# Kernel optimization log

Hardware: AMD Instinct MI355X
Metric: run time of the kernel (lower is better)

Reference implementation:

```python
import jax, jax.numpy as jnp
import numpy as np

EPS = 1e-8

def setup_inputs() -> dict:
    key = jax.random.key(0)
    student_output = jax.random.normal(key, (8192, 768), dtype=jnp.float32)
    return {"student_output": student_output}

def reference(student_output) -> jnp.ndarray:
    # KoLeo: -mean(log(nearest-neighbor euclidean distance + eps))
    x = student_output
    n = x.shape[0]
    sq = jnp.sum(x * x, axis=1)                      # [n]
    # squared pairwise distances via Gram matrix: ||xi||^2 + ||xj||^2 - 2 xi.xj
    d2 = sq[:, None] + sq[None, :] - 2.0 * (x @ x.T)  # [n, n]
    d2 = jnp.maximum(d2, 0.0)
    d2 = jnp.where(jnp.eye(n, dtype=bool), jnp.inf, d2)  # exclude self
    # sqrt is monotone, so min(sqrt(d2)) == sqrt(min(d2)) (matches torch cdist+min)
    min_dist = jnp.sqrt(jnp.min(d2, axis=1))          # [n]
    return -jnp.mean(jnp.log(min_dist + EPS))
```

## Files before the change

kernel.cpp:

```cpp
#include <hip/hip_runtime.h>
#include <hip/hip_bf16.h>
#include <math.h>

#define NROWS 8192
#define DIM   768
#define NKB   (DIM / 64)
#define FCH   8192
#define FPAN  (NKB * FCH)
#define NT128 (NROWS / 128)
#define NTILES (NT128 * (NT128 + 1) / 2)
#define PACK8B ((size_t)NT128 * FPAN)

typedef __attribute__((ext_vector_type(4))) float  f32x4;
typedef __attribute__((ext_vector_type(8))) __bf16 bf16x8;
typedef __attribute__((ext_vector_type(4))) __bf16 bf16x4;
typedef __attribute__((ext_vector_type(2))) long   longx2;

__device__ __forceinline__ void gload_lds16(const void* g, void* l) {
  __builtin_amdgcn_global_load_lds(
      (const __attribute__((address_space(1))) void*)g,
      (__attribute__((address_space(3))) void*)l, 16, 0, 0);
}

__global__ __launch_bounds__(256) void koleo_pack8(const float* __restrict__ X,
                                                   float* __restrict__ sq,
                                                   unsigned int* __restrict__ minbits,
                                                   char* __restrict__ xbf) {
  const int row  = blockIdx.x * 4 + (threadIdx.x >> 6);
  const int lane = threadIdx.x & 63;
  const int rb = row >> 7, r = row & 127;
  const float* xr = X + (size_t)row * DIM;
  float s = 0.f;
#pragma unroll
  for (int i = 0; i < 3; ++i) {
    const int c0 = lane * 4 + i * 256;
    f32x4 v = *(const f32x4*)(xr + c0);
    s += v.x * v.x + v.y * v.y + v.z * v.z + v.w * v.w;
    int pk = __builtin_amdgcn_cvt_pk_fp8_f32(v.x, v.y, 0, false);
    pk     = __builtin_amdgcn_cvt_pk_fp8_f32(v.z, v.w, pk, true);
    const int kb = c0 >> 6;
    const int c  = c0 & 63;
    const int ks = c >> 5;
    const int g  = (c >> 3) & 3;
    const int bb = c & 7;
    const int pos = g * 16 + ks * 8 + bb;
    const int off = (r * 64 + pos) ^ (((r >> 1) & 3) << 4);
    *(int*)(xbf + (size_t)rb * FPAN + (size_t)kb * FCH + off) = pk;
  }
#pragma unroll
  for (int m = 32; m >= 1; m >>= 1) s += __shfl_xor(s, m, 64);
  if (lane == 0) {
    sq[row]      = s;
    minbits[row] = 0x7F800000u;
  }
}

__global__ __launch_bounds__(256, 4) void koleo_tile8f(const char* __restrict__ xbf,
                                                       const float* __restrict__ sq,
                                                       unsigned int* __restrict__ minbits) {
  extern __shared__ char lds[];

  const int b = blockIdx.x;
  int ti, tj;
  if (b < 528) {
    int rem = b, rl = 32; ti = 0;
    while (rem >= rl) { rem -= rl; ++ti; --rl; }
    tj = ti + rem;
  } else if (b < 1552) {
    const int q = (b - 528) >> 8, rr = (b - 528) & 255;
    ti = rr >> 3; tj = 32 + q * 8 + (rr & 7);
  } else {
    int rem = b - 1552, rl = 32; ti = 32;
    while (rem >= rl) { rem -= rl; ++ti; --rl; }
    tj = ti + rem;
  }
  const int i0 = ti * 128, j0 = tj * 128;

  const int tid  = threadIdx.x;
  const int lane = tid & 63;
  const int wave = tid >> 6;
  const int wr   = wave >> 1;
  const int wc   = wave & 1;
  const int g16  = (lane >> 4) * 16;

  const char* pA = xbf + (size_t)ti * FPAN + wave * 1024 + lane * 16;
  const char* pB = xbf + (size_t)tj * FPAN + wave * 1024 + lane * 16;

  f32x4 acc[4][4] = {};

#pragma unroll
  for (int h = 0; h < 2; ++h) {
    gload_lds16(pA + h * 4096, lds +        h * 4096 + wave * 1024);
    gload_lds16(pB + h * 4096, lds + 8192 + h * 4096 + wave * 1024);
  }
  asm volatile("s_waitcnt vmcnt(0)" ::: "memory");
  __builtin_amdgcn_s_barrier();

  for (int t = 0; t < NKB; ++t) {
    char* buf  = lds + (t & 1) * 16384;
    char* nbuf = lds + ((t + 1) & 1) * 16384;
    const bool more = (t + 1 < NKB);

    if (more) {
      const char* sA = pA + (size_t)(t + 1) * FCH;
      const char* sB = pB + (size_t)(t + 1) * FCH;
#pragma unroll
      for (int h = 0; h < 2; ++h) {
        gload_lds16(sA + h * 4096, nbuf +        h * 4096 + wave * 1024);
        gload_lds16(sB + h * 4096, nbuf + 8192 + h * 4096 + wave * 1024);
      }
    }

    longx2 aP[4], bP[4];
#pragma unroll
    for (int m = 0; m < 4; ++m) {
      const int ra = wr * 64 + m * 16 + (lane & 15);
      aP[m] = *(const longx2*)(buf + ((ra * 64 + g16) ^ (((ra >> 1) & 3) << 4)));
      const int rb2 = wc * 64 + m * 16 + (lane & 15);
      bP[m] = *(const longx2*)(buf + 8192 + ((rb2 * 64 + g16) ^ (((rb2 >> 1) & 3) << 4)));
    }
#pragma unroll
    for (int ks = 0; ks < 2; ++ks)
#pragma unroll
      for (int m = 0; m < 4; ++m)
#pragma unroll
        for (int n = 0; n < 4; ++n)
          acc[m][n] = __builtin_amdgcn_mfma_f32_16x16x32_fp8_fp8(aP[m][ks], bP[n][ks], acc[m][n], 0, 0, 0);

    if (more) asm volatile("s_waitcnt vmcnt(0)" ::: "memory");
    __builtin_amdgcn_s_barrier();
  }

  const int cg = lane >> 4;
  const int cl = lane & 15;
  float sqj[4], colmin[4];
#pragma unroll
  for (int n = 0; n < 4; ++n) {
    sqj[n]    = sq[j0 + wc * 64 + n * 16 + cl];
    colmin[n] = INFINITY;
  }
#pragma unroll
  for (int m = 0; m < 4; ++m) {
#pragma unroll
    for (int r = 0; r < 4; ++r) {
      const int gi = i0 + wr * 64 + m * 16 + cg * 4 + r;
      const float si = sq[gi];
      float rowmin = INFINITY;
#pragma unroll
      for (int n = 0; n < 4; ++n) {
        const int gj = j0 + wc * 64 + n * 16 + cl;
        float d2 = si + sqj[n] - 2.0f * acc[m][n][r];
        d2 = fmaxf(d2, 0.0f);
        if (gi == gj) d2 = INFINITY;
        rowmin    = fminf(rowmin, d2);
        colmin[n] = fminf(colmin[n], d2);
      }
      rowmin = fminf(rowmin, __shfl_xor(rowmin, 1, 64));
      rowmin = fminf(rowmin, __shfl_xor(rowmin, 2, 64));
      rowmin = fminf(rowmin, __shfl_xor(rowmin, 4, 64));
      rowmin = fminf(rowmin, __shfl_xor(rowmin, 8, 64));
      if (cl == 0)
        atomicMin(minbits + gi, __float_as_uint(rowmin));
    }
  }
  if (ti != tj) {
#pragma unroll
    for (int n = 0; n < 4; ++n) {
      float cm = colmin[n];
      cm = fminf(cm, __shfl_xor(cm, 16, 64));
      cm = fminf(cm, __shfl_xor(cm, 32, 64));
      if (cg == 0)
        atomicMin(minbits + j0 + wc * 64 + n * 16 + cl, __float_as_uint(cm));
    }
  }
}

__global__ __launch_bounds__(256) void koleo_prep_fb(const float* __restrict__ X,
                                                     float* __restrict__ sq,
                                                     unsigned int* __restrict__ minbits) {
  const int row  = blockIdx.x * 4 + (threadIdx.x >> 6);
  const int lane = threadIdx.x & 63;
  const float* xr = X + (size_t)row * DIM;
  float s = 0.f;
#pragma unroll
  for (int i = 0; i < 3; ++i) {
    f32x4 v = *(const f32x4*)(xr + lane * 4 + i * 256);
    s += v.x * v.x + v.y * v.y + v.z * v.z + v.w * v.w;
  }
#pragma unroll
  for (int m = 32; m >= 1; m >>= 1) s += __shfl_xor(s, m, 64);
  if (lane == 0) { sq[row] = s; minbits[row] = 0x7F800000u; }
}

__global__ __launch_bounds__(256) void koleo_tile_fb(const float* __restrict__ X,
                                                     const float* __restrict__ sq,
                                                     unsigned int* __restrict__ minbits) {
  __shared__ __align__(16) char sA[16384];
  __shared__ __align__(16) char sB[16384];
  int rem = blockIdx.x, ti = 0, rowlen = NT128;
  while (rem >= rowlen) { rem -= rowlen; ++ti; --rowlen; }
  const int tj = ti + rem;
  const int i0 = ti * 128, j0 = tj * 128;
  const int tid = threadIdx.x, lane = tid & 63, wave = tid >> 6;
  const int wr = wave >> 1, wc = wave & 1;
  f32x4 acc[4][4] = {};
  for (int k0 = 0; k0 < DIM; k0 += 64) {
    __syncthreads();
#pragma unroll
    for (int it = 0; it < 8; ++it) {
      const int idx = tid + it * 256;
      const int r = idx >> 4, c4 = idx & 15;
      f32x4 va = *(const f32x4*)(X + (size_t)(i0 + r) * DIM + k0 + c4 * 4);
      f32x4 vb = *(const f32x4*)(X + (size_t)(j0 + r) * DIM + k0 + c4 * 4);
      bf16x4 ha, hb;
      ha[0] = (__bf16)va.x; ha[1] = (__bf16)va.y; ha[2] = (__bf16)va.z; ha[3] = (__bf16)va.w;
      hb[0] = (__bf16)vb.x; hb[1] = (__bf16)vb.y; hb[2] = (__bf16)vb.z; hb[3] = (__bf16)vb.w;
      int off = (r * 128 + c4 * 8) ^ ((r & 7) << 4);
      *(bf16x4*)(sA + off) = ha;
      *(bf16x4*)(sB + off) = hb;
    }
    __syncthreads();
#pragma unroll
    for (int ks = 0; ks < 2; ++ks) {
      bf16x8 af[4], bfr[4];
#pragma unroll
      for (int m = 0; m < 4; ++m) {
        const int ra = wr * 64 + m * 16 + (lane & 15);
        af[m]  = *(const bf16x8*)(sA + ((ra * 128 + ks * 64 + (lane >> 4) * 16) ^ ((ra & 7) << 4)));
        const int rb2 = wc * 64 + m * 16 + (lane & 15);
        bfr[m] = *(const bf16x8*)(sB + ((rb2 * 128 + ks * 64 + (lane >> 4) * 16) ^ ((rb2 & 7) << 4)));
      }
#pragma unroll
      for (int m = 0; m < 4; ++m)
#pragma unroll
        for (int n = 0; n < 4; ++n)
          acc[m][n] = __builtin_amdgcn_mfma_f32_16x16x32_bf16(af[m], bfr[n], acc[m][n], 0, 0, 0);
    }
  }
  const int cg = lane >> 4, cl = lane & 15;
  float sqj[4], colmin[4];
#pragma unroll
  for (int n = 0; n < 4; ++n) { sqj[n] = sq[j0 + wc * 64 + n * 16 + cl]; colmin[n] = INFINITY; }
#pragma unroll
  for (int m = 0; m < 4; ++m) {
#pragma unroll
    for (int r = 0; r < 4; ++r) {
      const int gi = i0 + wr * 64 + m * 16 + cg * 4 + r;
      const float si = sq[gi];
      float rowmin = INFINITY;
#pragma unroll
      for (int n = 0; n < 4; ++n) {
        const int gj = j0 + wc * 64 + n * 16 + cl;
        float d2 = si + sqj[n] - 2.0f * acc[m][n][r];
        d2 = fmaxf(d2, 0.0f);
        if (gi == gj) d2 = INFINITY;
        rowmin = fminf(rowmin, d2);
        colmin[n] = fminf(colmin[n], d2);
      }
      rowmin = fminf(rowmin, __shfl_xor(rowmin, 1, 64));
      rowmin = fminf(rowmin, __shfl_xor(rowmin, 2, 64));
      rowmin = fminf(rowmin, __shfl_xor(rowmin, 4, 64));
      rowmin = fminf(rowmin, __shfl_xor(rowmin, 8, 64));
      if (cl == 0) atomicMin(minbits + gi, __float_as_uint(rowmin));
    }
  }
  if (ti != tj) {
#pragma unroll
    for (int n = 0; n < 4; ++n) {
      float cm = colmin[n];
      cm = fminf(cm, __shfl_xor(cm, 16, 64));
      cm = fminf(cm, __shfl_xor(cm, 32, 64));
      if (cg == 0) atomicMin(minbits + j0 + wc * 64 + n * 16 + cl, __float_as_uint(cm));
    }
  }
}

__global__ __launch_bounds__(1024) void koleo_final(const unsigned int* __restrict__ minbits,
                                                    float* __restrict__ out) {
  __shared__ float wsum[16];
  float s = 0.f;
  for (int i = threadIdx.x; i < NROWS; i += 1024) {
    float d2 = __uint_as_float(minbits[i]);
    s += logf(sqrtf(d2) + 1e-8f);
  }
#pragma unroll
  for (int m = 32; m >= 1; m >>= 1) s += __shfl_xor(s, m, 64);
  const int wv = threadIdx.x >> 6, ln = threadIdx.x & 63;
  if (ln == 0) wsum[wv] = s;
  __syncthreads();
  if (wv == 0) {
    float t = (ln < 16) ? wsum[ln] : 0.f;
#pragma unroll
    for (int m = 8; m >= 1; m >>= 1) t += __shfl_xor(t, m, 64);
    if (ln == 0) out[0] = -t / (float)NROWS;
  }
}

extern "C" void kernel_launch(void* const* d_in, const int* in_sizes, int n_in,
                              void* d_out, int out_size, void* d_ws, size_t ws_size,
                              hipStream_t stream) {
  const float* X = (const float*)d_in[0];
  float* out = (float*)d_out;
  unsigned int* minbits = (unsigned int*)d_ws;
  float* sq = (float*)((char*)d_ws + NROWS * sizeof(unsigned int));
  char* xbf = (char*)d_ws + 65536;

  const size_t need = 65536 + PACK8B;
  if (ws_size >= need) {
    koleo_pack8<<<NROWS / 4, 256, 0, stream>>>(X, sq, minbits, xbf);
    koleo_tile8f<<<NTILES, 256, 32768, stream>>>(xbf, sq, minbits);
  } else {
    koleo_prep_fb<<<NROWS / 4, 256, 0, stream>>>(X, sq, minbits);
    koleo_tile_fb<<<NTILES, 256, 0, stream>>>(X, sq, minbits);
  }
  koleo_final<<<1, 1024, 0, stream>>>(minbits, out);
}
```

Before: 65.16 us.

## Enlarge symmetric Gram tiles to 256x256 with 16-wave blocks

```diff
diff --git a/kernel.cpp b/kernel.cpp
--- a/kernel.cpp
+++ b/kernel.cpp
@@ -8,7 +8,8 @@
 #define FCH   8192
 #define FPAN  (NKB * FCH)
 #define NT128 (NROWS / 128)
-#define NTILES (NT128 * (NT128 + 1) / 2)
+#define NT256 (NROWS / 256)
+#define NTIL2 (NT256 * (NT256 + 1) / 2)
 #define PACK8B ((size_t)NT128 * FPAN)
 
 typedef __attribute__((ext_vector_type(4))) float  f32x4;
@@ -55,69 +56,69 @@
   }
 }
 
-__global__ __launch_bounds__(256, 4) void koleo_tile8f(const char* __restrict__ xbf,
-                                                       const float* __restrict__ sq,
-                                                       unsigned int* __restrict__ minbits) {
+__global__ __launch_bounds__(1024, 4) void koleo_tile256(const char* __restrict__ xbf,
+                                                         const float* __restrict__ sq,
+                                                         unsigned int* __restrict__ minbits) {
   extern __shared__ char lds[];
 
   const int b = blockIdx.x;
   int ti, tj;
-  if (b < 528) {
-    int rem = b, rl = 32; ti = 0;
+  if (b < 136) {
+    int rem = b, rl = 16; ti = 0;
     while (rem >= rl) { rem -= rl; ++ti; --rl; }
     tj = ti + rem;
-  } else if (b < 1552) {
-    const int q = (b - 528) >> 8, rr = (b - 528) & 255;
-    ti = rr >> 3; tj = 32 + q * 8 + (rr & 7);
+  } else if (b < 392) {
+    const int q = (b - 136) >> 6, rr = (b - 136) & 63;
+    ti = rr >> 2; tj = 16 + q * 4 + (rr & 3);
   } else {
-    int rem = b - 1552, rl = 32; ti = 32;
+    int rem = b - 392, rl = 16; ti = 16;
     while (rem >= rl) { rem -= rl; ++ti; --rl; }
     tj = ti + rem;
   }
-  const int i0 = ti * 128, j0 = tj * 128;
+  const int i0 = ti * 256, j0 = tj * 256;
 
   const int tid  = threadIdx.x;
   const int lane = tid & 63;
   const int wave = tid >> 6;
-  const int wr   = wave >> 1;
-  const int wc   = wave & 1;
+  const int wr   = wave >> 2;
+  const int wc   = wave & 3;
   const int g16  = (lane >> 4) * 16;
 
-  const char* pA = xbf + (size_t)ti * FPAN + wave * 1024 + lane * 16;
-  const char* pB = xbf + (size_t)tj * FPAN + wave * 1024 + lane * 16;
+  const int sc   = wave >> 2;
+  const int spart= wave & 3;
+  const int srb  = (sc < 2) ? (2 * ti + sc) : (2 * tj + (sc - 2));
+  const char* sbase = xbf + (size_t)srb * FPAN + spart * 2048 + lane * 16;
+  const int sdst = sc * 8192 + spart * 2048;
 
   f32x4 acc[4][4] = {};
 
-#pragma unroll
-  for (int h = 0; h < 2; ++h) {
-    gload_lds16(pA + h * 4096, lds +        h * 4096 + wave * 1024);
-    gload_lds16(pB + h * 4096, lds + 8192 + h * 4096 + wave * 1024);
-  }
+  gload_lds16(sbase,        lds + sdst);
+  gload_lds16(sbase + 1024, lds + sdst + 1024);
   asm volatile("s_waitcnt vmcnt(0)" ::: "memory");
   __builtin_amdgcn_s_barrier();
 
   for (int t = 0; t < NKB; ++t) {
-    char* buf  = lds + (t & 1) * 16384;
-    char* nbuf = lds + ((t + 1) & 1) * 16384;
+    char* buf  = lds + (t & 1) * 32768;
+    char* nbuf = lds + ((t + 1) & 1) * 32768;
     const bool more = (t + 1 < NKB);
 
     if (more) {
-      const char* sA = pA + (size_t)(t + 1) * FCH;
-      const char* sB = pB + (size_t)(t + 1) * FCH;
-#pragma unroll
-      for (int h = 0; h < 2; ++h) {
-        gload_lds16(sA + h * 4096, nbuf +        h * 4096 + wave * 1024);
-        gload_lds16(sB + h * 4096, nbuf + 8192 + h * 4096 + wave * 1024);
-      }
+      const char* s = sbase + (size_t)(t + 1) * FCH;
+      gload_lds16(s,        nbuf + sdst);
+      gload_lds16(s + 1024, nbuf + sdst + 1024);
     }
 
     longx2 aP[4], bP[4];
 #pragma unroll
     for (int m = 0; m < 4; ++m) {
-      const int ra = wr * 64 + m * 16 + (lane & 15);
-      aP[m] = *(const longx2*)(buf + ((ra * 64 + g16) ^ (((ra >> 1) & 3) << 4)));
-      const int rb2 = wc * 64 + m * 16 + (lane & 15);
-      bP[m] = *(const longx2*)(buf + 8192 + ((rb2 * 64 + g16) ^ (((rb2 >> 1) & 3) << 4)));
+      const int r256 = wr * 64 + m * 16 + (lane & 15);
+      const int h = r256 >> 7, rr2 = r256 & 127;
+      aP[m] = *(const longx2*)(buf + h * 8192 +
+                ((rr2 * 64 + g16) ^ (((rr2 >> 1) & 3) << 4)));
+      const int c256 = wc * 64 + m * 16 + (lane & 15);
+      const int hb = c256 >> 7, rb2 = c256 & 127;
+      bP[m] = *(const longx2*)(buf + 16384 + hb * 8192 +
+                ((rb2 * 64 + g16) ^ (((rb2 >> 1) & 3) << 4)));
     }
 #pragma unroll
     for (int ks = 0; ks < 2; ++ks)
@@ -308,10 +309,10 @@
   const size_t need = 65536 + PACK8B;
   if (ws_size >= need) {
     koleo_pack8<<<NROWS / 4, 256, 0, stream>>>(X, sq, minbits, xbf);
-    koleo_tile8f<<<NTILES, 256, 32768, stream>>>(xbf, sq, minbits);
+    koleo_tile256<<<NTIL2, 1024, 65536, stream>>>(xbf, sq, minbits);
   } else {
     koleo_prep_fb<<<NROWS / 4, 256, 0, stream>>>(X, sq, minbits);
-    koleo_tile_fb<<<NTILES, 256, 0, stream>>>(X, sq, minbits);
+    koleo_tile_fb<<<NT128 * (NT128 + 1) / 2, 256, 0, stream>>>(X, sq, minbits);
   }
   koleo_final<<<1, 1024, 0, stream>>>(minbits, out);
 }
```

Result: slower. 84.98 us (+30.4%).

## Use 256x128 tiles with 512-thread blocks for the FP8 Gram kernel

Applied to the files above, without the earlier changes.

```diff
diff --git a/kernel.cpp b/kernel.cpp
--- a/kernel.cpp
+++ b/kernel.cpp
@@ -9,7 +9,9 @@
 #define FPAN  (NKB * FCH)
 #define NT128 (NROWS / 128)
 #define NTILES (NT128 * (NT128 + 1) / 2)
+#define NTIL3 1056
 #define PACK8B ((size_t)NT128 * FPAN)
+#define LDSB  49152
 
 typedef __attribute__((ext_vector_type(4))) float  f32x4;
 typedef __attribute__((ext_vector_type(8))) __bf16 bf16x8;
@@ -55,26 +57,27 @@
   }
 }
 
-__global__ __launch_bounds__(256, 4) void koleo_tile8f(const char* __restrict__ xbf,
-                                                       const float* __restrict__ sq,
-                                                       unsigned int* __restrict__ minbits) {
+__global__ __launch_bounds__(512, 4) void koleo_t256(const char* __restrict__ xbf,
+                                                     const float* __restrict__ sq,
+                                                     unsigned int* __restrict__ minbits) {
   extern __shared__ char lds[];
 
   const int b = blockIdx.x;
   int ti, tj;
-  if (b < 528) {
+  if (b < 272) {
     int rem = b, rl = 32; ti = 0;
-    while (rem >= rl) { rem -= rl; ++ti; --rl; }
-    tj = ti + rem;
-  } else if (b < 1552) {
-    const int q = (b - 528) >> 8, rr = (b - 528) & 255;
-    ti = rr >> 3; tj = 32 + q * 8 + (rr & 7);
+    while (rem >= rl) { rem -= rl; ++ti; rl -= 2; }
+    tj = 2 * ti + rem;
+  } else if (b < 784) {
+    const int idx = b - 272;
+    const int g = idx >> 7, rr = idx & 127;
+    ti = rr >> 3; tj = 32 + g * 8 + (rr & 7);
   } else {
-    int rem = b - 1552, rl = 32; ti = 32;
-    while (rem >= rl) { rem -= rl; ++ti; --rl; }
-    tj = ti + rem;
-  }
-  const int i0 = ti * 128, j0 = tj * 128;
+    int rem = b - 784, rl = 32; ti = 16;
+    while (rem >= rl) { rem -= rl; ++ti; rl -= 2; }
+    tj = 2 * ti + rem;
+  }
+  const int i0 = ti * 256, j0 = tj * 128;
 
   const int tid  = threadIdx.x;
   const int lane = tid & 63;
@@ -83,42 +86,48 @@
   const int wc   = wave & 1;
   const int g16  = (lane >> 4) * 16;
 
-  const char* pA = xbf + (size_t)ti * FPAN + wave * 1024 + lane * 16;
-  const char* pB = xbf + (size_t)tj * FPAN + wave * 1024 + lane * 16;
+  const char* ssrc[3];
+  int sdst[3];
+#pragma unroll
+  for (int k = 0; k < 3; ++k) {
+    const int s  = wave * 3 + k;
+    const int rb = (s < 16) ? (2 * ti + (s >> 3)) : tj;
+    const int of = (s < 16) ? ((s & 7) * 1024) : ((s - 16) * 1024);
+    ssrc[k] = xbf + (size_t)rb * FPAN + of + lane * 16;
+    sdst[k] = s * 1024;
+  }
 
   f32x4 acc[4][4] = {};
 
 #pragma unroll
-  for (int h = 0; h < 2; ++h) {
-    gload_lds16(pA + h * 4096, lds +        h * 4096 + wave * 1024);
-    gload_lds16(pB + h * 4096, lds + 8192 + h * 4096 + wave * 1024);
-  }
+  for (int k = 0; k < 3; ++k)
+    gload_lds16(ssrc[k], lds + sdst[k]);
   asm volatile("s_waitcnt vmcnt(0)" ::: "memory");
   __builtin_amdgcn_s_barrier();
 
   for (int t = 0; t < NKB; ++t) {
-    char* buf  = lds + (t & 1) * 16384;
-    char* nbuf = lds + ((t + 1) & 1) * 16384;
+    char* buf  = lds + (t & 1) * 24576;
+    char* nbuf = lds + ((t + 1) & 1) * 24576;
     const bool more = (t + 1 < NKB);
 
     if (more) {
-      const char* sA = pA + (size_t)(t + 1) * FCH;
-      const char* sB = pB + (size_t)(t + 1) * FCH;
-#pragma unroll
-      for (int h = 0; h < 2; ++h) {
-        gload_lds16(sA + h * 4096, nbuf +        h * 4096 + wave * 1024);
-        gload_lds16(sB + h * 4096, nbuf + 8192 + h * 4096 + wave * 1024);
-      }
+#pragma unroll
+      for (int k = 0; k < 3; ++k)
+        gload_lds16(ssrc[k] + (size_t)(t + 1) * FCH, nbuf + sdst[k]);
     }
 
     longx2 aP[4], bP[4];
 #pragma unroll
     for (int m = 0; m < 4; ++m) {
-      const int ra = wr * 64 + m * 16 + (lane & 15);
-      aP[m] = *(const longx2*)(buf + ((ra * 64 + g16) ^ (((ra >> 1) & 3) << 4)));
-      const int rb2 = wc * 64 + m * 16 + (lane & 15);
-      bP[m] = *(const longx2*)(buf + 8192 + ((rb2 * 64 + g16) ^ (((rb2 >> 1) & 3) << 4)));
-    }
+      const int r256 = wr * 64 + m * 16 + (lane & 15);
+      const int h = r256 >> 7, rr2 = r256 & 127;
+      aP[m] = *(const longx2*)(buf + h * 8192 +
+                ((rr2 * 64 + g16) ^ (((rr2 >> 1) & 3) << 4)));
+      const int c128 = wc * 64 + m * 16 + (lane & 15);
+      bP[m] = *(const longx2*)(buf + 16384 +
+                ((c128 * 64 + g16) ^ (((c128 >> 1) & 3) << 4)));
+    }
+    __builtin_amdgcn_s_setprio(1);
 #pragma unroll
     for (int ks = 0; ks < 2; ++ks)
 #pragma unroll
@@ -126,6 +135,7 @@
 #pragma unroll
         for (int n = 0; n < 4; ++n)
           acc[m][n] = __builtin_amdgcn_mfma_f32_16x16x32_fp8_fp8(aP[m][ks], bP[n][ks], acc[m][n], 0, 0, 0);
+    __builtin_amdgcn_s_setprio(0);
 
     if (more) asm volatile("s_waitcnt vmcnt(0)" ::: "memory");
     __builtin_amdgcn_s_barrier();
@@ -163,15 +173,13 @@
         atomicMin(minbits + gi, __float_as_uint(rowmin));
     }
   }
-  if (ti != tj) {
-#pragma unroll
-    for (int n = 0; n < 4; ++n) {
-      float cm = colmin[n];
-      cm = fminf(cm, __shfl_xor(cm, 16, 64));
-      cm = fminf(cm, __shfl_xor(cm, 32, 64));
-      if (cg == 0)
-        atomicMin(minbits + j0 + wc * 64 + n * 16 + cl, __float_as_uint(cm));
-    }
+#pragma unroll
+  for (int n = 0; n < 4; ++n) {
+    float cm = colmin[n];
+    cm = fminf(cm, __shfl_xor(cm, 16, 64));
+    cm = fminf(cm, __shfl_xor(cm, 32, 64));
+    if (cg == 0)
+      atomicMin(minbits + j0 + wc * 64 + n * 16 + cl, __float_as_uint(cm));
   }
 }
 
@@ -308,7 +316,7 @@
   const size_t need = 65536 + PACK8B;
   if (ws_size >= need) {
     koleo_pack8<<<NROWS / 4, 256, 0, stream>>>(X, sq, minbits, xbf);
-    koleo_tile8f<<<NTILES, 256, 32768, stream>>>(xbf, sq, minbits);
+    koleo_t256<<<NTIL3, 512, LDSB, stream>>>(xbf, sq, minbits);
   } else {
     koleo_prep_fb<<<NROWS / 4, 256, 0, stream>>>(X, sq, minbits);
     koleo_tile_fb<<<NTILES, 256, 0, stream>>>(X, sq, minbits);
```

Result: slower. 66.48 us (+2.0%).
